# Kernel tuning notes

Measured on AMD Instinct MI355X. Metric: run time of the kernel, lower is better.

Reference implementation:

```python
import jax, jax.numpy as jnp
import numpy as np

TOPK = 2
ALPHA = 0.1
EPS = 1e-20


def setup_inputs() -> dict:
    key = jax.random.key(0)
    k1, k2 = jax.random.split(key)
    hidden_states = jax.random.normal(k1, (4, 4096, 2048), dtype=jnp.float32)
    # kaiming_uniform_(a=sqrt(5)) on [E, H] ~ U(-1/sqrt(H), 1/sqrt(H))
    bound = 1.0 / np.sqrt(2048)
    weight = jax.random.uniform(k2, (64, 2048), dtype=jnp.float32, minval=-bound, maxval=bound)
    return {"hidden_states": hidden_states, "weight": weight}


def reference(hidden_states, weight):
    B, S, H = hidden_states.shape
    E = weight.shape[0]
    x = hidden_states.reshape(-1, H)                      # [B*S, H]
    logits = jnp.einsum('th,eh->te', x, weight)           # [B*S, E]
    scores = jax.nn.softmax(logits, axis=-1)
    topk_weight, topk_idx = jax.lax.top_k(scores, TOPK)   # [B*S, K]
    # norm_topk_prob
    topk_weight = topk_weight / (topk_weight.sum(axis=-1, keepdims=True) + EPS)
    # seq_aux load-balancing loss (training path)
    idx = topk_idx.reshape(B, S * TOPK)                   # [B, S*K]
    ce = jnp.zeros((B, E), dtype=scores.dtype)
    ce = ce.at[jnp.arange(B)[:, None], idx].add(1.0)      # scatter_add counts
    ce = ce * (E / (S * TOPK))
    expert_scores = scores.reshape(B, S, E).mean(axis=1)  # [B, E]
    aux_loss = (ce * expert_scores).sum(axis=1).mean() * ALPHA
    return topk_idx, topk_weight, aux_loss
```

## Files before the change

### kernel.cpp

```cpp
#include <hip/hip_runtime.h>

#define TAU 8e-3f

typedef __attribute__((ext_vector_type(8))) short bf16x8;
typedef __attribute__((ext_vector_type(4))) float f32x4;
typedef __attribute__((ext_vector_type(4))) unsigned int u32x4;

#define LOGITS_OFF 262144
#define ACCUM_OFF (262144 + 4194304)

#define RNE16(f) \
  ((unsigned short)((__float_as_uint(f) + 0x7fffu + ((__float_as_uint(f) >> 16) & 1u)) >> 16))

#define CVTPK(dst, a, b) \
  asm("v_cvt_pk_bf16_f32 %0, %1, %2" : "=v"(dst) : "v"(a), "v"(b))

__global__ __launch_bounds__(256) void wconv(const float* __restrict__ W,
                                             unsigned short* __restrict__ Wswz,
                                             float* __restrict__ accum) {
  int t = blockIdx.x * 256 + threadIdx.x;
  int g = t >> 12, rem = t & 4095;
  int ks = rem >> 6, lane = rem & 63;
  int fm = lane & 15, kg = lane >> 4;
  const float* src = W + (size_t)(g * 16 + fm) * 2048 + ks * 32 + kg * 8;
  float4 a = *(const float4*)src;
  float4 b = *(const float4*)(src + 4);
  ushort4 lo = make_ushort4(RNE16(a.x), RNE16(a.y), RNE16(a.z), RNE16(a.w));
  ushort4 hi = make_ushort4(RNE16(b.x), RNE16(b.y), RNE16(b.z), RNE16(b.w));
  unsigned short* dst = Wswz + (size_t)t * 8;
  *(ushort4*)dst = lo;
  *(ushort4*)(dst + 4) = hi;
  if (blockIdx.x == 0) {
    accum[threadIdx.x] = 0.f;
    accum[256 + threadIdx.x] = 0.f;
    if (threadIdx.x == 0) ((unsigned*)accum)[512] = 0u;
  }
}

__global__ __launch_bounds__(512, 8) void gate_gemm(
    const float* __restrict__ x, const unsigned short* __restrict__ Wswz,
    float* __restrict__ logits) {
  __shared__ float part[8][16][68];

  const int tid = threadIdx.x;
  const int lane = tid & 63;
  const int w = __builtin_amdgcn_readfirstlane(tid >> 6);
  const int fm = lane & 15;
  const int kg = lane >> 4;
  const int tok0 = blockIdx.x * 16;

  const float* xr = x + (size_t)(tok0 + fm) * 2048 + w * 256 + kg * 8;
  const bf16x8* wsw = (const bf16x8*)Wswz + lane;

  f32x4 acc[4];
#pragma unroll
  for (int g = 0; g < 4; ++g) acc[g] = (f32x4){0.f, 0.f, 0.f, 0.f};

#pragma unroll
  for (int it = 0; it < 8; ++it) {
    const int ks = w * 8 + it;
    float4 p0 = *(const float4*)(xr + it * 32);
    float4 p1 = *(const float4*)(xr + it * 32 + 4);
    bf16x8 b0 = wsw[(0 * 64 + ks) * 64];
    bf16x8 b1 = wsw[(1 * 64 + ks) * 64];
    bf16x8 b2 = wsw[(2 * 64 + ks) * 64];
    bf16x8 b3 = wsw[(3 * 64 + ks) * 64];
    unsigned u0, u1, u2, u3;
    CVTPK(u0, p0.x, p0.y);
    CVTPK(u1, p0.z, p0.w);
    CVTPK(u2, p1.x, p1.y);
    CVTPK(u3, p1.z, p1.w);
    u32x4 uu = (u32x4){u0, u1, u2, u3};
    bf16x8 a = __builtin_bit_cast(bf16x8, uu);
    acc[0] = __builtin_amdgcn_mfma_f32_16x16x32_bf16(a, b0, acc[0], 0, 0, 0);
    acc[1] = __builtin_amdgcn_mfma_f32_16x16x32_bf16(a, b1, acc[1], 0, 0, 0);
    acc[2] = __builtin_amdgcn_mfma_f32_16x16x32_bf16(a, b2, acc[2], 0, 0, 0);
    acc[3] = __builtin_amdgcn_mfma_f32_16x16x32_bf16(a, b3, acc[3], 0, 0, 0);
  }

#pragma unroll
  for (int g = 0; g < 4; ++g)
#pragma unroll
    for (int r = 0; r < 4; ++r)
      part[w][kg * 4 + r][g * 16 + fm] = acc[g][r];
  __syncthreads();

#pragma unroll
  for (int p = tid; p < 1024; p += 512) {
    int t = p >> 6, e = p & 63;
    float s = part[0][t][e];
#pragma unroll
    for (int ww = 1; ww < 8; ++ww) s += part[ww][t][e];
    logits[(size_t)(tok0 + t) * 64 + e] = s;
  }
}

__global__ __launch_bounds__(1024) void gate_top(
    const float* __restrict__ x, const float* __restrict__ Wf,
    const float* __restrict__ logits, float* __restrict__ out,
    float* __restrict__ accum) {
  __shared__ float sm[16][64];
  __shared__ float cn[16][64];

  const int tid = threadIdx.x;
  const int lane = tid & 63;
  const int w = tid >> 6;
  const int tok0 = blockIdx.x * 64;
  const int b = blockIdx.x >> 6;

  float ssum = 0.f;
  float cnt = 0.f;

  for (int i = 0; i < 4; ++i) {
    const int tok = tok0 + w * 4 + i;
    float v = logits[(size_t)tok * 64 + lane];

    float m1 = v; int i1 = lane;
#pragma unroll
    for (int o = 32; o; o >>= 1) {
      float ov = __shfl_xor(m1, o, 64);
      int oi = __shfl_xor(i1, o, 64);
      if (ov > m1 || (ov == m1 && oi < i1)) { m1 = ov; i1 = oi; }
    }
    float v2 = (lane == i1) ? -3e38f : v;
    float m2 = v2; int i2 = lane;
#pragma unroll
    for (int o = 32; o; o >>= 1) {
      float ov = __shfl_xor(m2, o, 64);
      int oi = __shfl_xor(i2, o, 64);
      if (ov > m2 || (ov == m2 && oi < i2)) { m2 = ov; i2 = oi; }
    }
    float m3 = (lane == i1 || lane == i2) ? -3e38f : v;
#pragma unroll
    for (int o = 32; o; o >>= 1) m3 = fmaxf(m3, __shfl_xor(m3, o, 64));

    if ((m1 - m2 < TAU) || (m2 - m3 < TAU)) {
      unsigned long long cand = __ballot(v >= m2 - TAU);
      const float* xr2 = x + (size_t)tok * 2048 + lane * 32;
      while (cand) {
        int e = __ffsll(cand) - 1;
        cand &= cand - 1;
        const float* wr = Wf + (size_t)e * 2048 + lane * 32;
        float s = 0.f;
#pragma unroll
        for (int kk = 0; kk < 32; kk += 8) {
          float4 u0 = *(const float4*)(xr2 + kk);
          float4 w0 = *(const float4*)(wr + kk);
          float4 u1 = *(const float4*)(xr2 + kk + 4);
          float4 w1 = *(const float4*)(wr + kk + 4);
          s += u0.x * w0.x + u0.y * w0.y + u0.z * w0.z + u0.w * w0.w +
               u1.x * w1.x + u1.y * w1.y + u1.z * w1.z + u1.w * w1.w;
        }
#pragma unroll
        for (int o = 32; o; o >>= 1) s += __shfl_xor(s, o, 64);
        if (lane == e) v = s;
      }
      m1 = v; i1 = lane;
#pragma unroll
      for (int o = 32; o; o >>= 1) {
        float ov = __shfl_xor(m1, o, 64);
        int oi = __shfl_xor(i1, o, 64);
        if (ov > m1 || (ov == m1 && oi < i1)) { m1 = ov; i1 = oi; }
      }
      v2 = (lane == i1) ? -3e38f : v;
      m2 = v2; i2 = lane;
#pragma unroll
      for (int o = 32; o; o >>= 1) {
        float ov = __shfl_xor(m2, o, 64);
        int oi = __shfl_xor(i2, o, 64);
        if (ov > m2 || (ov == m2 && oi < i2)) { m2 = ov; i2 = oi; }
      }
    }

    float ez = __expf(v - m1);
    float Z = ez;
#pragma unroll
    for (int o = 32; o; o >>= 1) Z += __shfl_xor(Z, o, 64);
    float iz = 1.f / Z;
    float p1 = iz;
    float p2 = __expf(m2 - m1) * iz;
    float dn = 1.f / (p1 + p2 + 1e-20f);
    if (lane == 0) {
      size_t tg = (size_t)tok;
      out[tg * 2 + 0] = (float)i1;
      out[tg * 2 + 1] = (float)i2;
      out[32768 + tg * 2 + 0] = p1 * dn;
      out[32768 + tg * 2 + 1] = p2 * dn;
    }
    ssum += ez * iz;
    cnt += (float)((lane == i1) + (lane == i2));
  }

  sm[w][lane] = ssum;
  cn[w][lane] = cnt;
  __syncthreads();

  if (tid < 64) {
    float s = 0.f, c = 0.f;
#pragma unroll
    for (int ww = 0; ww < 16; ++ww) { s += sm[ww][tid]; c += cn[ww][tid]; }
    atomicAdd(&accum[b * 64 + tid], s);
    atomicAdd(&accum[256 + b * 64 + tid], c);

    __threadfence();
    unsigned old = 0;
    if (tid == 0) old = atomicAdd((unsigned*)accum + 512, 1u);
    old = (unsigned)__shfl((int)old, 0, 64);
    if (old == 255u) {
      __threadfence();
      float tot = 0.f;
#pragma unroll
      for (int bb = 0; bb < 4; ++bb) {
        float ss = atomicAdd(&accum[bb * 64 + tid], 0.f);
        float cc = atomicAdd(&accum[256 + bb * 64 + tid], 0.f);
        tot += cc * (1.f / 128.f) * (ss * (1.f / 4096.f));
      }
#pragma unroll
      for (int o = 32; o; o >>= 1) tot += __shfl_xor(tot, o, 64);
      if (tid == 0) out[65536] = 0.025f * tot;
    }
  }
}

extern "C" void kernel_launch(void* const* d_in, const int* in_sizes, int n_in,
                              void* d_out, int out_size, void* d_ws, size_t ws_size,
                              hipStream_t stream) {
  const float* x = (const float*)d_in[0];
  const float* Wf = (const float*)d_in[1];
  float* out = (float*)d_out;
  unsigned short* Wswz = (unsigned short*)d_ws;
  float* logits = (float*)((char*)d_ws + LOGITS_OFF);
  float* accum = (float*)((char*)d_ws + ACCUM_OFF);
  wconv<<<64, 256, 0, stream>>>(Wf, Wswz, accum);
  gate_gemm<<<1024, 512, 0, stream>>>(x, Wswz, logits);
  gate_top<<<256, 1024, 0, stream>>>(x, Wf, logits, out, accum);
}
```

Baseline: 221.7 us.

## Stage x through double-buffered LDS with direct global-to-LDS loads in gate GEMM

The gate GEMM now uses 256-thread blocks where each wave owns 16 experts over the full K, instead of splitting K across 8 waves and reducing partials in shared memory. Activation tiles are streamed into a double-buffered, XOR-swizzled LDS buffer with global_load_lds, prefetching the next chunk while MFMAs run on the current one. This removes the cross-wave partial-sum reduction and overlaps memory with compute. In exchange it adds a barrier per step, and per-wave MFMA chains become long serial dependencies on a single accumulator.

```diff
diff --git a/kernel.cpp b/kernel.cpp
--- a/kernel.cpp
+++ b/kernel.cpp
@@ -14,6 +14,11 @@
 
 #define CVTPK(dst, a, b) \
   asm("v_cvt_pk_bf16_f32 %0, %1, %2" : "=v"(dst) : "v"(a), "v"(b))
+
+#define GL16(gp, lp)                                                          \
+  __builtin_amdgcn_global_load_lds(                                           \
+      (const __attribute__((address_space(1))) unsigned int*)(gp),            \
+      (__attribute__((address_space(3))) unsigned int*)(lp), 16, 0, 0)
 
 __global__ __launch_bounds__(256) void wconv(const float* __restrict__ W,
                                              unsigned short* __restrict__ Wswz,
@@ -37,10 +42,10 @@
   }
 }
 
-__global__ __launch_bounds__(512, 8) void gate_gemm(
+__global__ __launch_bounds__(256, 4) void gate_gemm(
     const float* __restrict__ x, const unsigned short* __restrict__ Wswz,
     float* __restrict__ logits) {
-  __shared__ float part[8][16][68];
+  __shared__ float __attribute__((aligned(16))) xlds[2][2048];
 
   const int tid = threadIdx.x;
   const int lane = tid & 63;
@@ -49,50 +54,67 @@
   const int kg = lane >> 4;
   const int tok0 = blockIdx.x * 16;
 
-  const float* xr = x + (size_t)(tok0 + fm) * 2048 + w * 256 + kg * 8;
+  const float* src0;
+  const float* src1;
+  {
+    int p0 = tid, q0 = p0 ^ ((p0 >> 5) & 7);
+    int p1 = 256 + tid, q1 = p1 ^ ((p1 >> 5) & 7);
+    src0 = x + (size_t)(tok0 + (q0 >> 5)) * 2048 + (q0 & 31) * 4;
+    src1 = x + (size_t)(tok0 + (q1 >> 5)) * 2048 + (q1 & 31) * 4;
+  }
+  float* lds_d0 = &xlds[0][tid * 4];
+  float* lds_d1 = &xlds[0][1024 + tid * 4];
+
+  const char* lb0 = (const char*)xlds + fm * 512 + (((kg * 2 + 0) ^ (fm & 7)) * 16);
+  const char* lb1 = (const char*)xlds + fm * 512 + (((kg * 2 + 1) ^ (fm & 7)) * 16);
+
   const bf16x8* wsw = (const bf16x8*)Wswz + lane;
 
-  f32x4 acc[4];
-#pragma unroll
-  for (int g = 0; g < 4; ++g) acc[g] = (f32x4){0.f, 0.f, 0.f, 0.f};
-
-#pragma unroll
-  for (int it = 0; it < 8; ++it) {
-    const int ks = w * 8 + it;
-    float4 p0 = *(const float4*)(xr + it * 32);
-    float4 p1 = *(const float4*)(xr + it * 32 + 4);
-    bf16x8 b0 = wsw[(0 * 64 + ks) * 64];
-    bf16x8 b1 = wsw[(1 * 64 + ks) * 64];
-    bf16x8 b2 = wsw[(2 * 64 + ks) * 64];
-    bf16x8 b3 = wsw[(3 * 64 + ks) * 64];
-    unsigned u0, u1, u2, u3;
-    CVTPK(u0, p0.x, p0.y);
-    CVTPK(u1, p0.z, p0.w);
-    CVTPK(u2, p1.x, p1.y);
-    CVTPK(u3, p1.z, p1.w);
-    u32x4 uu = (u32x4){u0, u1, u2, u3};
-    bf16x8 a = __builtin_bit_cast(bf16x8, uu);
-    acc[0] = __builtin_amdgcn_mfma_f32_16x16x32_bf16(a, b0, acc[0], 0, 0, 0);
-    acc[1] = __builtin_amdgcn_mfma_f32_16x16x32_bf16(a, b1, acc[1], 0, 0, 0);
-    acc[2] = __builtin_amdgcn_mfma_f32_16x16x32_bf16(a, b2, acc[2], 0, 0, 0);
-    acc[3] = __builtin_amdgcn_mfma_f32_16x16x32_bf16(a, b3, acc[3], 0, 0, 0);
-  }
-
-#pragma unroll
-  for (int g = 0; g < 4; ++g)
-#pragma unroll
-    for (int r = 0; r < 4; ++r)
-      part[w][kg * 4 + r][g * 16 + fm] = acc[g][r];
+  f32x4 acc = (f32x4){0.f, 0.f, 0.f, 0.f};
+
+#define STEP(BUF, S, DO_STAGE)                                               \
+  {                                                                          \
+    bf16x8 b0 = wsw[(w * 64 + (S) * 4 + 0) * 64];                            \
+    bf16x8 b1 = wsw[(w * 64 + (S) * 4 + 1) * 64];                            \
+    bf16x8 b2 = wsw[(w * 64 + (S) * 4 + 2) * 64];                            \
+    bf16x8 b3 = wsw[(w * 64 + (S) * 4 + 3) * 64];                            \
+    if (DO_STAGE) {                                                          \
+      GL16(src0 + ((S) + 1) * 128, lds_d0 + (1 - (BUF)) * 2048);             \
+      GL16(src1 + ((S) + 1) * 128, lds_d1 + (1 - (BUF)) * 2048);             \
+    }                                                                        \
+    _Pragma("unroll")                                                        \
+    for (int ks = 0; ks < 4; ++ks) {                                         \
+      float4 lo = *(const float4*)(lb0 + (BUF)*8192 + ks * 128);             \
+      float4 hi = *(const float4*)(lb1 + (BUF)*8192 + ks * 128);             \
+      unsigned u0, u1, u2, u3;                                               \
+      CVTPK(u0, lo.x, lo.y);                                                 \
+      CVTPK(u1, lo.z, lo.w);                                                 \
+      CVTPK(u2, hi.x, hi.y);                                                 \
+      CVTPK(u3, hi.z, hi.w);                                                 \
+      u32x4 uu = (u32x4){u0, u1, u2, u3};                                    \
+      bf16x8 a = __builtin_bit_cast(bf16x8, uu);                             \
+      bf16x8 bb = (ks == 0) ? b0 : (ks == 1) ? b1 : (ks == 2) ? b2 : b3;     \
+      acc = __builtin_amdgcn_mfma_f32_16x16x32_bf16(a, bb, acc, 0, 0, 0);    \
+    }                                                                        \
+    __syncthreads();                                                         \
+  }
+
+  GL16(src0, lds_d0);
+  GL16(src1, lds_d1);
   __syncthreads();
 
-#pragma unroll
-  for (int p = tid; p < 1024; p += 512) {
-    int t = p >> 6, e = p & 63;
-    float s = part[0][t][e];
-#pragma unroll
-    for (int ww = 1; ww < 8; ++ww) s += part[ww][t][e];
-    logits[(size_t)(tok0 + t) * 64 + e] = s;
-  }
+#pragma unroll 1
+  for (int s = 0; s < 14; s += 2) {
+    STEP(0, s, true)
+    STEP(1, s + 1, true)
+  }
+  STEP(0, 14, true)
+  STEP(1, 15, false)
+#undef STEP
+
+#pragma unroll
+  for (int r = 0; r < 4; ++r)
+    logits[(size_t)(tok0 + kg * 4 + r) * 64 + w * 16 + fm] = acc[r];
 }
 
 __global__ __launch_bounds__(1024) void gate_top(
@@ -232,6 +254,6 @@
   float* logits = (float*)((char*)d_ws + LOGITS_OFF);
   float* accum = (float*)((char*)d_ws + ACCUM_OFF);
   wconv<<<64, 256, 0, stream>>>(Wf, Wswz, accum);
-  gate_gemm<<<1024, 512, 0, stream>>>(x, Wswz, logits);
+  gate_gemm<<<1024, 256, 0, stream>>>(x, Wswz, logits);
   gate_top<<<256, 1024, 0, stream>>>(x, Wf, logits, out, accum);
 }
```

After: 218.3 us. Within noise of the previous version (-1.5%).
